# Performance work log

Hardware: AMD Instinct MI355X
Metric: run time of the kernel (lower is better)

Reference implementation:

```python
import jax, jax.numpy as jnp
import numpy as np

FULL_SCALE = 128
TOPK = 8
R = 0.5


def setup_inputs() -> dict:
    key = jax.random.key(0)
    ks = jax.random.split(key, 6)
    B, Na, Nb, D = 4, 8192, 8192, 256
    return {
        "a_feats": jax.random.normal(ks[0], (B, Na, D), jnp.float32),
        "b_feats": jax.random.normal(ks[1], (B, Nb, D), jnp.float32),
        "coords_a": jax.random.randint(ks[2], (B, Na, 3), 0, 2048, jnp.int32),
        "coords_b": jax.random.randint(ks[3], (B, Nb, 3), 0, 2048, jnp.int32),
        "w1": jax.random.normal(ks[4], (D, 2 * D), jnp.float32) / np.sqrt(2 * D),
        "b1": jnp.zeros((D,), jnp.float32),
        "w2": jax.random.normal(ks[5], (D, D), jnp.float32) / np.sqrt(D),
        "b2": jnp.zeros((D,), jnp.float32),
    }


def _cli_one(af, bf, ca, cb, w1, b1, w2, b2):
    # af:[Na,D] bf:[Nb,D] ca:[Na,3] cb:[Nb,3] (float coords, already //16)
    # torch.cdist (euclidean) / full_scale
    d2 = (jnp.sum(ca * ca, 1)[:, None] + jnp.sum(cb * cb, 1)[None, :]
          - 2.0 * ca @ cb.T)
    dist = jnp.sqrt(jnp.maximum(d2, 0.0)) / FULL_SCALE  # [Na, Nb]
    neg_d, idx = jax.lax.top_k(-dist, TOPK)             # smallest k distances
    dw = R - jnp.clip(-neg_d, 0.0, R)                   # [Na, k]
    nb = bf[idx]                                        # gather [Na, k, D]
    x = jnp.concatenate([nb, af[:, None, :] - nb], axis=-1)  # [Na, k, 2D]
    h = jax.nn.relu(jnp.einsum('nkf,df->nkd', x, w1) + b1) * dw[..., None]
    o = jnp.einsum('nkd,ed->nke', h, w2) + b2           # [Na, k, D]
    return jnp.sum(o, axis=1)                           # [Na, D]


def reference(a_feats, b_feats, coords_a, coords_b, w1, b1, w2, b2):
    ca = (coords_a // 16).astype(jnp.float32)
    cb = (coords_b // 16).astype(jnp.float32)
    fuse = jax.vmap(lambda af, bf, x, y: _cli_one(af, bf, x, y, w1, b1, w2, b2))(
        a_feats, b_feats, ca, cb)
    # ME.cat(a, tmp): concatenate features along channel dim
    return jnp.concatenate([a_feats, fuse], axis=-1)  # [B, Na, 2D]
```

## Files before the change

### kernel.cpp

```cpp
#include <hip/hip_runtime.h>
#include <math.h>

typedef short short8_t __attribute__((ext_vector_type(8)));
typedef __bf16 bf16x8_t __attribute__((ext_vector_type(8)));
typedef float f32x4_t __attribute__((ext_vector_type(4)));

__device__ __forceinline__ float bf2f(unsigned short u) {
  unsigned v = ((unsigned)u) << 16;
  return __builtin_bit_cast(float, v);
}
__device__ __forceinline__ unsigned short f2bf(float f) {
  unsigned x = __builtin_bit_cast(unsigned, f);
  x += 0x7fffu + ((x >> 16) & 1u);
  return (unsigned short)(x >> 16);
}

#define NA 8192
#define NB 8192
#define NBATCH 4
#define DIM 256
#define NPTS (NBATCH * NA)
#define NCELL 2048
#define SUBL 8

__device__ __forceinline__ void kins(unsigned k[8], unsigned x) {
  unsigned c = x < k[7] ? x : k[7];
#pragma unroll
  for (int i = 6; i >= 0; i--) {
    unsigned hi = k[i] > c ? k[i] : c;
    c = k[i] < c ? k[i] : c;
    k[i + 1] = hi;
  }
  k[0] = c;
}

__global__ __launch_bounds__(256) void prep_weights(
    const float* __restrict__ w1, const float* __restrict__ w2,
    unsigned short* __restrict__ Wdiff, unsigned short* __restrict__ Wb,
    unsigned short* __restrict__ W2b, unsigned* __restrict__ bcnt,
    unsigned* __restrict__ acnt, unsigned* __restrict__ failcnt) {
  int d = blockIdx.x, t = threadIdx.x;
  float wa = w1[d * 512 + t];
  float wb = w1[d * 512 + 256 + t];
  Wdiff[d * 256 + t] = f2bf(wa - wb);
  Wb[d * 256 + t] = f2bf(wb);
  W2b[d * 256 + t] = f2bf(w2[d * 256 + t]);
  if (d < 8) {
    int i = d * 256 + t;
    bcnt[i] = 0;
    acnt[i] = 0;
    if (i == 0) *failcnt = 0;
  }
}

__global__ __launch_bounds__(256) void pack_count_ab(
    const int* __restrict__ coords_b, const int* __restrict__ coords_a,
    unsigned* __restrict__ bpk, unsigned* __restrict__ apk,
    unsigned* __restrict__ bcnt, unsigned* __restrict__ acnt) {
  int gi = blockIdx.x * 256 + threadIdx.x;
  const int isA = gi >= NPTS;
  const int i = gi & (NPTS - 1);
  const int* __restrict__ coords = isA ? coords_a : coords_b;
  unsigned* __restrict__ pk = isA ? apk : bpk;
  unsigned* __restrict__ cnt = isA ? acnt : bcnt;
  int x = (coords[(size_t)i * 3 + 0] >> 4) & 127;
  int y = (coords[(size_t)i * 3 + 1] >> 4) & 127;
  int z = (coords[(size_t)i * 3 + 2] >> 4) & 127;
  pk[i] = (unsigned)(x | (y << 7) | (z << 14));
  int cid = ((i >> 13) << 9) | ((x >> 4) << 6) | ((y >> 4) << 3) | (z >> 4);
  atomicAdd(cnt + cid, 1u);
}

__global__ __launch_bounds__(256) void scan_cells(
    const unsigned* __restrict__ bcnt, const unsigned* __restrict__ acnt,
    unsigned* __restrict__ boff, unsigned* __restrict__ aoff,
    unsigned* __restrict__ bcur, unsigned* __restrict__ acur) {
  __shared__ unsigned p[256];
  const int t = threadIdx.x;
  for (int tab = 0; tab < 2; tab++) {
    const unsigned* cnt = tab ? acnt : bcnt;
    unsigned* off = tab ? aoff : boff;
    unsigned* cur = tab ? acur : bcur;
    unsigned loc[8], sum = 0;
#pragma unroll
    for (int k = 0; k < 8; k++) { loc[k] = sum; sum += cnt[t * 8 + k]; }
    p[t] = sum;
    __syncthreads();
    for (int d = 1; d < 256; d <<= 1) {
      unsigned v = (t >= d) ? p[t - d] : 0u;
      __syncthreads();
      p[t] += v;
      __syncthreads();
    }
    unsigned base = (t == 0) ? 0u : p[t - 1];
#pragma unroll
    for (int k = 0; k < 8; k++) {
      unsigned o = base + loc[k];
      off[t * 8 + k] = o;
      cur[t * 8 + k] = o;
    }
    if (t == 255) off[2048] = base + sum;
    __syncthreads();
  }
}

__global__ __launch_bounds__(256) void scatter_ab(
    const unsigned* __restrict__ bpk, const unsigned* __restrict__ apk,
    unsigned* __restrict__ bcur, unsigned* __restrict__ acur,
    uint2* __restrict__ bout, uint2* __restrict__ aout) {
  int gi = blockIdx.x * 256 + threadIdx.x;
  const int isA = gi >= NPTS;
  const int i = gi & (NPTS - 1);
  const unsigned* __restrict__ pk = isA ? apk : bpk;
  unsigned* __restrict__ cur = isA ? acur : bcur;
  uint2* __restrict__ out = isA ? aout : bout;
  unsigned v = pk[i];
  int cx = (v & 127) >> 4, cy = ((v >> 7) & 127) >> 4, cz = ((v >> 14) & 127) >> 4;
  int cid = ((i >> 13) << 9) | (cx << 6) | (cy << 3) | cz;
  unsigned pos = atomicAdd(cur + cid, 1u);
  out[pos] = make_uint2(v, (unsigned)(i & 8191));
}

#define LDT 72
template <int F32IN>
__device__ __forceinline__ void gemm64_body(
    int rowblk, const void* __restrict__ Ain, const short* __restrict__ W,
    float* __restrict__ Cf, unsigned short* __restrict__ Cb,
    const float* __restrict__ bias, float bias_scale, int c_stride,
    int c_coloff, float* __restrict__ copyout, short* As, short* Bs) {
  const int tid = threadIdx.x;
  const int row0 = rowblk * 64;
  const int w = tid >> 6, lane = tid & 63;
  const int wn = w * 64;
  f32x4_t acc[4][4] = {};
  for (int k0 = 0; k0 < 256; k0 += 64) {
    if (F32IN) {
      const float* Af = (const float*)Ain;
#pragma unroll
      for (int i = 0; i < 2; i++) {
        int c = tid + 256 * i;
        int r = c >> 3, kc = (c & 7) * 8;
        const float* src = Af + (size_t)(row0 + r) * 256 + k0 + kc;
        float4 v0 = *(const float4*)src;
        float4 v1 = *(const float4*)(src + 4);
        short8_t vb;
        vb[0] = (short)f2bf(v0.x); vb[1] = (short)f2bf(v0.y);
        vb[2] = (short)f2bf(v0.z); vb[3] = (short)f2bf(v0.w);
        vb[4] = (short)f2bf(v1.x); vb[5] = (short)f2bf(v1.y);
        vb[6] = (short)f2bf(v1.z); vb[7] = (short)f2bf(v1.w);
        *(short8_t*)(As + r * LDT + kc) = vb;
        if (copyout) {
          float4* dst = (float4*)(copyout + (size_t)(row0 + r) * 512 + k0 + kc);
          dst[0] = v0;
          dst[1] = v1;
        }
      }
    } else {
      const short* Ab = (const short*)Ain;
#pragma unroll
      for (int i = 0; i < 2; i++) {
        int c = tid + 256 * i;
        int r = c >> 3, kc = (c & 7) * 8;
        *(short8_t*)(As + r * LDT + kc) =
            *(const short8_t*)(Ab + (size_t)(row0 + r) * 256 + k0 + kc);
      }
    }
#pragma unroll
    for (int i = 0; i < 8; i++) {
      int c = tid + 256 * i;
      int r = c >> 3, kc = (c & 7) * 8;
      *(short8_t*)(Bs + r * LDT + kc) =
          *(const short8_t*)(W + (size_t)r * 256 + k0 + kc);
    }
    __syncthreads();
#pragma unroll
    for (int kk = 0; kk < 64; kk += 32) {
      const int kof = kk + (lane >> 4) * 8;
      bf16x8_t af[4], bfr[4];
#pragma unroll
      for (int i = 0; i < 4; i++) {
        af[i] = __builtin_bit_cast(bf16x8_t,
            *(const short8_t*)(As + (i * 16 + (lane & 15)) * LDT + kof));
        bfr[i] = __builtin_bit_cast(bf16x8_t,
            *(const short8_t*)(Bs + (wn + i * 16 + (lane & 15)) * LDT + kof));
      }
#pragma unroll
      for (int i = 0; i < 4; i++)
#pragma unroll
        for (int j = 0; j < 4; j++)
          acc[i][j] = __builtin_amdgcn_mfma_f32_16x16x32_bf16(
              af[i], bfr[j], acc[i][j], 0, 0, 0);
    }
    __syncthreads();
  }
#pragma unroll
  for (int i = 0; i < 4; i++) {
    int row = row0 + i * 16 + ((lane >> 4) * 4);
#pragma unroll
    for (int j = 0; j < 4; j++) {
      int col = wn + j * 16 + (lane & 15);
      float bv = bias ? bias[col] * bias_scale : 0.f;
#pragma unroll
      for (int r = 0; r < 4; r++) {
        float v = acc[i][j][r] + bv;
        size_t off = (size_t)(row + r) * c_stride + c_coloff + col;
        if (Cf) Cf[off] = v;
        else Cb[off] = f2bf(v);
      }
    }
  }
}

__global__ __launch_bounds__(256, 3) void gemm_ab(
    const float* __restrict__ a_feats, const float* __restrict__ b_feats,
    const short* __restrict__ Wb16, const short* __restrict__ Wdiff,
    unsigned short* __restrict__ Pa, unsigned short* __restrict__ Pb,
    const float* __restrict__ b1, float* __restrict__ outp) {
  __shared__ __attribute__((aligned(16))) short As[64 * LDT];
  __shared__ __attribute__((aligned(16))) short Bs[256 * LDT];
  const int nb = NPTS / 64;
  const int isB = blockIdx.x >= nb;
  const int rowblk = isB ? (blockIdx.x - nb) : blockIdx.x;
  const float* Af = isB ? b_feats : a_feats;
  const short* W = isB ? Wdiff : Wb16;
  unsigned short* P = isB ? Pb : Pa;
  const float* bias = isB ? nullptr : b1;
  float* copy = isB ? nullptr : outp;
  gemm64_body<1>(rowblk, (const void*)Af, W, nullptr, P, bias, 1.0f, 256, 0,
                 copy, As, Bs);
}

__global__ __launch_bounds__(256, 3) void gemm_h(
    const short* __restrict__ Hb, const short* __restrict__ W2b,
    float* __restrict__ outp, const float* __restrict__ b2) {
  __shared__ __attribute__((aligned(16))) short As[64 * LDT];
  __shared__ __attribute__((aligned(16))) short Bs[256 * LDT];
  gemm64_body<0>(blockIdx.x, (const void*)Hb, W2b, outp, nullptr, b2, 8.0f,
                 512, 256, nullptr, As, Bs);
}

__global__ __launch_bounds__(256) void topk_bins(
    const unsigned* __restrict__ boff, const uint2* __restrict__ bcj,
    const uint2* __restrict__ acj, int* __restrict__ idxb,
    float* __restrict__ dwb, unsigned* __restrict__ failcnt,
    unsigned* __restrict__ faillist) {
  const int tid = blockIdx.x * 256 + threadIdx.x;
  const int t = tid / SUBL;
  const int sub = tid & (SUBL - 1);
  const uint2 av = acj[t];
  const int batch = t >> 13;
  const int ax = av.x & 127, ay = (av.x >> 7) & 127, az = (av.x >> 14) & 127;
  const int cx = ax >> 4, cy = ay >> 4, cz = az >> 4;
  const int xlo = max(cx - 1, 0), xhi = min(cx + 1, 7);
  const int ylo = max(cy - 1, 0), yhi = min(cy + 1, 7);
  const int zlo = max(cz - 1, 0), zhi1 = min(cz + 1, 7) + 1;
  unsigned k[8];
#pragma unroll
  for (int s = 0; s < 8; s++) k[s] = 0xFFFFFFF8u + s;
  for (int nx = xlo; nx <= xhi; nx++) {
    for (int ny = ylo; ny <= yhi; ny++) {
      const int cb = (batch << 9) | (nx << 6) | (ny << 3);
      const int gs = (int)boff[cb + zlo];
      const int ge = (int)boff[cb + zhi1];
      for (int i = gs + sub; i < ge; i += SUBL) {
        const uint2 b = bcj[i];
        const int dx = ax - (int)(b.x & 127);
        const int dy = ay - (int)((b.x >> 7) & 127);
        const int dz = az - (int)((b.x >> 14) & 127);
        const unsigned d2 = (unsigned)(__mul24(dx, dx) + __mul24(dy, dy) +
                                       __mul24(dz, dz));
        kins(k, (d2 << 13) | b.y);
      }
    }
  }
  const int lane = threadIdx.x & 63;
#pragma unroll
  for (int half = 1; half < SUBL; half <<= 1) {
    unsigned o[8];
#pragma unroll
    for (int s = 0; s < 8; s++)
      o[s] = (unsigned)__shfl((int)k[s], lane ^ half, 64);
#pragma unroll
    for (int s = 0; s < 8; s++) kins(k, o[s]);
  }
  if (sub == 0) {
    const int g = (batch << 13) | (int)av.y;
#pragma unroll
    for (int s = 0; s < 8; s++) {
      unsigned key = k[s];
      idxb[(size_t)g * 8 + s] = (int)(key & 8191u);
      float dist = sqrtf((float)(key >> 13)) * (1.0f / 128.0f);
      dwb[(size_t)g * 8 + s] = 0.5f - fminf(dist, 0.5f);
    }
    if (k[7] >= (289u << 13)) {
      unsigned fp = atomicAdd(failcnt, 1u);
      faillist[fp] = (unsigned)g;
    }
  }
}

__global__ __launch_bounds__(256) void topk_fallback(
    const unsigned* __restrict__ failcnt, const unsigned* __restrict__ faillist,
    const uint2* __restrict__ bcj, const unsigned* __restrict__ apk,
    int* __restrict__ idxb, float* __restrict__ dwb) {
  __shared__ unsigned sk[4 * 8];
  const int tid = threadIdx.x;
  const int wv = tid >> 6, lane = tid & 63;
  const unsigned nf = *failcnt;
  for (unsigned fi = blockIdx.x; fi < nf; fi += gridDim.x) {
    const unsigned g = faillist[fi];
    const int batch = (int)(g >> 13);
    const unsigned av = apk[g];
    const int ax = av & 127, ay = (av >> 7) & 127, az = (av >> 14) & 127;
    const uint2* pb = bcj + ((size_t)batch << 13);
    unsigned k[8];
#pragma unroll
    for (int s = 0; s < 8; s++) k[s] = 0xFFFFFFF8u + s;
#pragma unroll 8
    for (int i = tid; i < NB; i += 256) {
      const uint2 b = pb[i];
      const int dx = ax - (int)(b.x & 127);
      const int dy = ay - (int)((b.x >> 7) & 127);
      const int dz = az - (int)((b.x >> 14) & 127);
      const unsigned d2 = (unsigned)(__mul24(dx, dx) + __mul24(dy, dy) +
                                     __mul24(dz, dz));
      kins(k, (d2 << 13) | b.y);
    }
#pragma unroll
    for (int half = 32; half >= 1; half >>= 1) {
      unsigned o[8];
#pragma unroll
      for (int s = 0; s < 8; s++)
        o[s] = (unsigned)__shfl((int)k[s], lane ^ half, 64);
#pragma unroll
      for (int s = 0; s < 8; s++) kins(k, o[s]);
    }
    if (lane == 0) {
#pragma unroll
      for (int s = 0; s < 8; s++) sk[wv * 8 + s] = k[s];
    }
    __syncthreads();
    if (tid == 0) {
#pragma unroll
      for (int w = 1; w < 4; w++)
#pragma unroll
        for (int s = 0; s < 8; s++) kins(k, sk[w * 8 + s]);
#pragma unroll
      for (int s = 0; s < 8; s++) {
        unsigned key = k[s];
        idxb[(size_t)g * 8 + s] = (int)(key & 8191u);
        float dist = sqrtf((float)(key >> 13)) * (1.0f / 128.0f);
        dwb[(size_t)g * 8 + s] = 0.5f - fminf(dist, 0.5f);
      }
    }
    __syncthreads();
  }
}

__global__ __launch_bounds__(256) void fuse_kernel(
    const unsigned short* __restrict__ Pa, const unsigned short* __restrict__ Pb,
    const uint2* __restrict__ acj, const int* __restrict__ idxb,
    const float* __restrict__ dwb, unsigned short* __restrict__ H) {
  const int t = blockIdx.x * 4 + (threadIdx.x >> 6);
  const int lane = threadIdx.x & 63;
  const int batch = t >> 13;
  const uint2 av = acj[t];
  const int g = (batch << 13) | (int)av.y;
  const size_t fo = (size_t)g * 256 + lane * 4;
  ushort4 pav = *(const ushort4*)(Pa + fo);
  const float pa0 = bf2f(pav.x), pa1 = bf2f(pav.y), pa2 = bf2f(pav.z),
              pa3 = bf2f(pav.w);
  float h0 = 0.f, h1 = 0.f, h2 = 0.f, h3 = 0.f;
  const size_t bbase = (size_t)(batch << 13) * 256;
#pragma unroll
  for (int k = 0; k < 8; k++) {
    const int j = idxb[(size_t)g * 8 + k];
    const float w = dwb[(size_t)g * 8 + k];
    const ushort4 pbv =
        *(const ushort4*)(Pb + bbase + (size_t)j * 256 + lane * 4);
    h0 += fmaxf(pa0 + bf2f(pbv.x), 0.f) * w;
    h1 += fmaxf(pa1 + bf2f(pbv.y), 0.f) * w;
    h2 += fmaxf(pa2 + bf2f(pbv.z), 0.f) * w;
    h3 += fmaxf(pa3 + bf2f(pbv.w), 0.f) * w;
  }
  ushort4 hv;
  hv.x = f2bf(h0); hv.y = f2bf(h1); hv.z = f2bf(h2); hv.w = f2bf(h3);
  *(ushort4*)(H + fo) = hv;
}

extern "C" void kernel_launch(void* const* d_in, const int* in_sizes, int n_in,
                              void* d_out, int out_size, void* d_ws,
                              size_t ws_size, hipStream_t stream) {
  const float* a_feats = (const float*)d_in[0];
  const float* b_feats = (const float*)d_in[1];
  const int* coords_a = (const int*)d_in[2];
  const int* coords_b = (const int*)d_in[3];
  const float* w1 = (const float*)d_in[4];
  const float* b1 = (const float*)d_in[5];
  const float* w2 = (const float*)d_in[6];
  const float* b2 = (const float*)d_in[7];
  float* outp = (float*)d_out;

  char* p = (char*)d_ws;
  auto take = [&](size_t bytes) {
    char* r = p;
    p += (bytes + 255) & ~(size_t)255;
    return r;
  };
  unsigned short* Pa = (unsigned short*)take((size_t)NPTS * DIM * 2);
  unsigned short* Pb = (unsigned short*)take((size_t)NPTS * DIM * 2);
  unsigned short* Hb = (unsigned short*)take((size_t)NPTS * DIM * 2);
  int* idxb = (int*)take((size_t)NPTS * 8 * 4);
  float* dwb = (float*)take((size_t)NPTS * 8 * 4);
  unsigned* bpk = (unsigned*)take((size_t)NPTS * 4);
  unsigned* apk = (unsigned*)take((size_t)NPTS * 4);
  unsigned* bcnt = (unsigned*)take(NCELL * 4);
  unsigned* acnt = (unsigned*)take(NCELL * 4);
  unsigned* bcur = (unsigned*)take(NCELL * 4);
  unsigned* acur = (unsigned*)take(NCELL * 4);
  unsigned* boff = (unsigned*)take((NCELL + 1) * 4);
  unsigned* aoff = (unsigned*)take((NCELL + 1) * 4);
  uint2* bcj = (uint2*)take((size_t)NPTS * 8);
  uint2* acj = (uint2*)take((size_t)NPTS * 8);
  unsigned* failcnt = (unsigned*)take(256);
  unsigned* faillist = (unsigned*)take((size_t)NPTS * 4);
  unsigned short* Wdiff = (unsigned short*)take(256 * 256 * 2);
  unsigned short* Wb16 = (unsigned short*)take(256 * 256 * 2);
  unsigned short* W2b = (unsigned short*)take(256 * 256 * 2);

  prep_weights<<<256, 256, 0, stream>>>(w1, w2, Wdiff, Wb16, W2b, bcnt, acnt,
                                        failcnt);
  pack_count_ab<<<2 * NPTS / 256, 256, 0, stream>>>(coords_b, coords_a, bpk,
                                                    apk, bcnt, acnt);
  scan_cells<<<1, 256, 0, stream>>>(bcnt, acnt, boff, aoff, bcur, acur);
  scatter_ab<<<2 * NPTS / 256, 256, 0, stream>>>(bpk, apk, bcur, acur, bcj,
                                                 acj);

  gemm_ab<<<2 * NPTS / 64, 256, 0, stream>>>(a_feats, b_feats,
                                             (const short*)Wb16,
                                             (const short*)Wdiff, Pa, Pb, b1,
                                             outp);

  topk_bins<<<NPTS * SUBL / 256, 256, 0, stream>>>(boff, bcj, acj, idxb, dwb,
                                                   failcnt, faillist);
  topk_fallback<<<256, 256, 0, stream>>>(failcnt, faillist, bcj, apk, idxb,
                                         dwb);

  fuse_kernel<<<NPTS / 4, 256, 0, stream>>>(Pa, Pb, acj, idxb, dwb, Hb);

  gemm_h<<<NPTS / 64, 256, 0, stream>>>((const short*)Hb, (const short*)W2b,
                                        outp, b2);
}
```

Baseline: 227.0 us.

## Double-buffer A tile with register prefetch and read weights directly from global

The GEMM body now prefetches the next 64-wide K slice of A into registers while the current one is consumed, writing into two alternating LDS buffers, so one barrier per iteration is dropped. The weight tile is no longer staged in shared memory; each wave loads its B fragments straight from global/L2. LDS per block falls sharply and launch bounds no longer force three blocks per CU, which should raise occupancy. The cost is uncoalesced-ish per-lane global weight loads inside the MFMA loop and higher register pressure from the prefetch buffers.

```diff
diff --git a/kernel.cpp b/kernel.cpp
--- a/kernel.cpp
+++ b/kernel.cpp
@@ -127,51 +127,56 @@
     int rowblk, const void* __restrict__ Ain, const short* __restrict__ W,
     float* __restrict__ Cf, unsigned short* __restrict__ Cb,
     const float* __restrict__ bias, float bias_scale, int c_stride,
-    int c_coloff, float* __restrict__ copyout, short* As, short* Bs) {
+    int c_coloff, float* __restrict__ copyout, short* As) {
   const int tid = threadIdx.x;
   const int row0 = rowblk * 64;
   const int w = tid >> 6, lane = tid & 63;
   const int wn = w * 64;
+  const int r0 = tid >> 3, kc = (tid & 7) * 8;
+  const int r1 = r0 + 32;
+  const short* wbase = W + (size_t)(wn + (lane & 15)) * 256 + (lane >> 4) * 8;
   f32x4_t acc[4][4] = {};
+
+  float4 p00, p01, p10, p11;
+  short8_t pb0, pb1;
+  const float* Af = (const float*)Ain;
+  const short* Ab = (const short*)Ain;
+#define LOADA(K0)                                                   \
+  if (F32IN) {                                                      \
+    const float* s0 = Af + (size_t)(row0 + r0) * 256 + (K0) + kc;   \
+    const float* s1 = Af + (size_t)(row0 + r1) * 256 + (K0) + kc;   \
+    p00 = *(const float4*)s0; p01 = *(const float4*)(s0 + 4);       \
+    p10 = *(const float4*)s1; p11 = *(const float4*)(s1 + 4);       \
+  } else {                                                          \
+    pb0 = *(const short8_t*)(Ab + (size_t)(row0 + r0) * 256 + (K0) + kc); \
+    pb1 = *(const short8_t*)(Ab + (size_t)(row0 + r1) * 256 + (K0) + kc); \
+  }
+  LOADA(0)
   for (int k0 = 0; k0 < 256; k0 += 64) {
+    short* Ac = As + ((k0 >> 6) & 1) * (64 * LDT);
     if (F32IN) {
-      const float* Af = (const float*)Ain;
-#pragma unroll
-      for (int i = 0; i < 2; i++) {
-        int c = tid + 256 * i;
-        int r = c >> 3, kc = (c & 7) * 8;
-        const float* src = Af + (size_t)(row0 + r) * 256 + k0 + kc;
-        float4 v0 = *(const float4*)src;
-        float4 v1 = *(const float4*)(src + 4);
-        short8_t vb;
-        vb[0] = (short)f2bf(v0.x); vb[1] = (short)f2bf(v0.y);
-        vb[2] = (short)f2bf(v0.z); vb[3] = (short)f2bf(v0.w);
-        vb[4] = (short)f2bf(v1.x); vb[5] = (short)f2bf(v1.y);
-        vb[6] = (short)f2bf(v1.z); vb[7] = (short)f2bf(v1.w);
-        *(short8_t*)(As + r * LDT + kc) = vb;
-        if (copyout) {
-          float4* dst = (float4*)(copyout + (size_t)(row0 + r) * 512 + k0 + kc);
-          dst[0] = v0;
-          dst[1] = v1;
-        }
+      short8_t vb;
+      vb[0] = (short)f2bf(p00.x); vb[1] = (short)f2bf(p00.y);
+      vb[2] = (short)f2bf(p00.z); vb[3] = (short)f2bf(p00.w);
+      vb[4] = (short)f2bf(p01.x); vb[5] = (short)f2bf(p01.y);
+      vb[6] = (short)f2bf(p01.z); vb[7] = (short)f2bf(p01.w);
+      *(short8_t*)(Ac + r0 * LDT + kc) = vb;
+      vb[0] = (short)f2bf(p10.x); vb[1] = (short)f2bf(p10.y);
+      vb[2] = (short)f2bf(p10.z); vb[3] = (short)f2bf(p10.w);
+      vb[4] = (short)f2bf(p11.x); vb[5] = (short)f2bf(p11.y);
+      vb[6] = (short)f2bf(p11.z); vb[7] = (short)f2bf(p11.w);
+      *(short8_t*)(Ac + r1 * LDT + kc) = vb;
+      if (copyout) {
+        float4* d0 = (float4*)(copyout + (size_t)(row0 + r0) * 512 + k0 + kc);
+        d0[0] = p00; d0[1] = p01;
+        float4* d1 = (float4*)(copyout + (size_t)(row0 + r1) * 512 + k0 + kc);
+        d1[0] = p10; d1[1] = p11;
       }
     } else {
-      const short* Ab = (const short*)Ain;
-#pragma unroll
-      for (int i = 0; i < 2; i++) {
-        int c = tid + 256 * i;
-        int r = c >> 3, kc = (c & 7) * 8;
-        *(short8_t*)(As + r * LDT + kc) =
-            *(const short8_t*)(Ab + (size_t)(row0 + r) * 256 + k0 + kc);
-      }
-    }
-#pragma unroll
-    for (int i = 0; i < 8; i++) {
-      int c = tid + 256 * i;
-      int r = c >> 3, kc = (c & 7) * 8;
-      *(short8_t*)(Bs + r * LDT + kc) =
-          *(const short8_t*)(W + (size_t)r * 256 + k0 + kc);
-    }
+      *(short8_t*)(Ac + r0 * LDT + kc) = pb0;
+      *(short8_t*)(Ac + r1 * LDT + kc) = pb1;
+    }
+    if (k0 < 192) { LOADA(k0 + 64) }
     __syncthreads();
 #pragma unroll
     for (int kk = 0; kk < 64; kk += 32) {
@@ -180,9 +185,9 @@
 #pragma unroll
       for (int i = 0; i < 4; i++) {
         af[i] = __builtin_bit_cast(bf16x8_t,
-            *(const short8_t*)(As + (i * 16 + (lane & 15)) * LDT + kof));
+            *(const short8_t*)(Ac + (i * 16 + (lane & 15)) * LDT + kof));
         bfr[i] = __builtin_bit_cast(bf16x8_t,
-            *(const short8_t*)(Bs + (wn + i * 16 + (lane & 15)) * LDT + kof));
+            *(const short8_t*)(wbase + (size_t)i * 16 * 256 + k0 + kk));
       }
 #pragma unroll
       for (int i = 0; i < 4; i++)
@@ -191,8 +196,8 @@
           acc[i][j] = __builtin_amdgcn_mfma_f32_16x16x32_bf16(
               af[i], bfr[j], acc[i][j], 0, 0, 0);
     }
-    __syncthreads();
-  }
+  }
+#undef LOADA
 #pragma unroll
   for (int i = 0; i < 4; i++) {
     int row = row0 + i * 16 + ((lane >> 4) * 4);
@@ -211,13 +216,12 @@
   }
 }
 
-__global__ __launch_bounds__(256, 3) void gemm_ab(
+__global__ __launch_bounds__(256) void gemm_ab(
     const float* __restrict__ a_feats, const float* __restrict__ b_feats,
     const short* __restrict__ Wb16, const short* __restrict__ Wdiff,
     unsigned short* __restrict__ Pa, unsigned short* __restrict__ Pb,
     const float* __restrict__ b1, float* __restrict__ outp) {
-  __shared__ __attribute__((aligned(16))) short As[64 * LDT];
-  __shared__ __attribute__((aligned(16))) short Bs[256 * LDT];
+  __shared__ __attribute__((aligned(16))) short As[2 * 64 * LDT];
   const int nb = NPTS / 64;
   const int isB = blockIdx.x >= nb;
   const int rowblk = isB ? (blockIdx.x - nb) : blockIdx.x;
@@ -227,16 +231,15 @@
   const float* bias = isB ? nullptr : b1;
   float* copy = isB ? nullptr : outp;
   gemm64_body<1>(rowblk, (const void*)Af, W, nullptr, P, bias, 1.0f, 256, 0,
-                 copy, As, Bs);
-}
-
-__global__ __launch_bounds__(256, 3) void gemm_h(
+                 copy, As);
+}
+
+__global__ __launch_bounds__(256) void gemm_h(
     const short* __restrict__ Hb, const short* __restrict__ W2b,
     float* __restrict__ outp, const float* __restrict__ b2) {
-  __shared__ __attribute__((aligned(16))) short As[64 * LDT];
-  __shared__ __attribute__((aligned(16))) short Bs[256 * LDT];
+  __shared__ __attribute__((aligned(16))) short As[2 * 64 * LDT];
   gemm64_body<0>(blockIdx.x, (const void*)Hb, W2b, outp, nullptr, b2, 8.0f,
-                 512, 256, nullptr, As, Bs);
+                 512, 256, nullptr, As);
 }
 
 __global__ __launch_bounds__(256) void topk_bins(
```

After: 227.7 us. About the same (+0.3%).

## Replace LDS-tiled GEMMs with per-wave 16-row strips streaming weights from global

Applied to the files above, without the earlier changes.

Both GEMMs now drop shared-memory tiling and barriers. Each wave owns a 16-row strip, keeps its full K=256 A fragment in registers, and reads the 256x256 bf16 weight fragments directly from global memory (L1/L2) for all 16 output column tiles. This removes LDS staging, __syncthreads and occupancy limits from shared memory. In exchange every wave re-reads the whole weight matrix from cache, so there is far less reuse per loaded weight and more register pressure.

```diff
diff --git a/kernel.cpp b/kernel.cpp
--- a/kernel.cpp
+++ b/kernel.cpp
@@ -121,122 +121,96 @@
   out[pos] = make_uint2(v, (unsigned)(i & 8191));
 }
 
-#define LDT 72
 template <int F32IN>
-__device__ __forceinline__ void gemm64_body(
-    int rowblk, const void* __restrict__ Ain, const short* __restrict__ W,
+__device__ __forceinline__ void gemm_strip(
+    int strip, const void* __restrict__ Ain, const short* __restrict__ W,
     float* __restrict__ Cf, unsigned short* __restrict__ Cb,
     const float* __restrict__ bias, float bias_scale, int c_stride,
-    int c_coloff, float* __restrict__ copyout, short* As, short* Bs) {
-  const int tid = threadIdx.x;
-  const int row0 = rowblk * 64;
-  const int w = tid >> 6, lane = tid & 63;
-  const int wn = w * 64;
-  f32x4_t acc[4][4] = {};
-  for (int k0 = 0; k0 < 256; k0 += 64) {
-    if (F32IN) {
-      const float* Af = (const float*)Ain;
-#pragma unroll
-      for (int i = 0; i < 2; i++) {
-        int c = tid + 256 * i;
-        int r = c >> 3, kc = (c & 7) * 8;
-        const float* src = Af + (size_t)(row0 + r) * 256 + k0 + kc;
-        float4 v0 = *(const float4*)src;
-        float4 v1 = *(const float4*)(src + 4);
-        short8_t vb;
-        vb[0] = (short)f2bf(v0.x); vb[1] = (short)f2bf(v0.y);
-        vb[2] = (short)f2bf(v0.z); vb[3] = (short)f2bf(v0.w);
-        vb[4] = (short)f2bf(v1.x); vb[5] = (short)f2bf(v1.y);
-        vb[6] = (short)f2bf(v1.z); vb[7] = (short)f2bf(v1.w);
-        *(short8_t*)(As + r * LDT + kc) = vb;
-        if (copyout) {
-          float4* dst = (float4*)(copyout + (size_t)(row0 + r) * 512 + k0 + kc);
-          dst[0] = v0;
-          dst[1] = v1;
-        }
+    int c_coloff, float* __restrict__ copyout) {
+  const int lane = threadIdx.x & 63;
+  const int r = lane & 15, g = lane >> 4;
+  const int row0 = strip * 16;
+  const float* Af = (const float*)Ain;
+  const short* Ab = (const short*)Ain;
+  bf16x8_t a[8];
+  if (F32IN) {
+#pragma unroll
+    for (int k = 0; k < 8; k++) {
+      const float* s = Af + (size_t)(row0 + r) * 256 + k * 32 + g * 8;
+      float4 v0 = *(const float4*)s;
+      float4 v1 = *(const float4*)(s + 4);
+      short8_t vb;
+      vb[0] = (short)f2bf(v0.x); vb[1] = (short)f2bf(v0.y);
+      vb[2] = (short)f2bf(v0.z); vb[3] = (short)f2bf(v0.w);
+      vb[4] = (short)f2bf(v1.x); vb[5] = (short)f2bf(v1.y);
+      vb[6] = (short)f2bf(v1.z); vb[7] = (short)f2bf(v1.w);
+      a[k] = __builtin_bit_cast(bf16x8_t, vb);
+      if (copyout) {
+        float4* d = (float4*)(copyout + (size_t)(row0 + r) * 512 + k * 32 + g * 8);
+        d[0] = v0;
+        d[1] = v1;
       }
-    } else {
-      const short* Ab = (const short*)Ain;
-#pragma unroll
-      for (int i = 0; i < 2; i++) {
-        int c = tid + 256 * i;
-        int r = c >> 3, kc = (c & 7) * 8;
-        *(short8_t*)(As + r * LDT + kc) =
-            *(const short8_t*)(Ab + (size_t)(row0 + r) * 256 + k0 + kc);
-      }
-    }
-#pragma unroll
-    for (int i = 0; i < 8; i++) {
-      int c = tid + 256 * i;
-      int r = c >> 3, kc = (c & 7) * 8;
-      *(short8_t*)(Bs + r * LDT + kc) =
-          *(const short8_t*)(W + (size_t)r * 256 + k0 + kc);
-    }
-    __syncthreads();
-#pragma unroll
-    for (int kk = 0; kk < 64; kk += 32) {
-      const int kof = kk + (lane >> 4) * 8;
-      bf16x8_t af[4], bfr[4];
-#pragma unroll
-      for (int i = 0; i < 4; i++) {
-        af[i] = __builtin_bit_cast(bf16x8_t,
-            *(const short8_t*)(As + (i * 16 + (lane & 15)) * LDT + kof));
-        bfr[i] = __builtin_bit_cast(bf16x8_t,
-            *(const short8_t*)(Bs + (wn + i * 16 + (lane & 15)) * LDT + kof));
-      }
-#pragma unroll
-      for (int i = 0; i < 4; i++)
-#pragma unroll
-        for (int j = 0; j < 4; j++)
-          acc[i][j] = __builtin_amdgcn_mfma_f32_16x16x32_bf16(
-              af[i], bfr[j], acc[i][j], 0, 0, 0);
-    }
-    __syncthreads();
-  }
-#pragma unroll
-  for (int i = 0; i < 4; i++) {
-    int row = row0 + i * 16 + ((lane >> 4) * 4);
-#pragma unroll
-    for (int j = 0; j < 4; j++) {
-      int col = wn + j * 16 + (lane & 15);
-      float bv = bias ? bias[col] * bias_scale : 0.f;
-#pragma unroll
-      for (int r = 0; r < 4; r++) {
-        float v = acc[i][j][r] + bv;
-        size_t off = (size_t)(row + r) * c_stride + c_coloff + col;
-        if (Cf) Cf[off] = v;
-        else Cb[off] = f2bf(v);
-      }
-    }
-  }
-}
-
-__global__ __launch_bounds__(256, 3) void gemm_ab(
+    }
+  } else {
+#pragma unroll
+    for (int k = 0; k < 8; k++)
+      a[k] = __builtin_bit_cast(bf16x8_t,
+          *(const short8_t*)(Ab + (size_t)(row0 + r) * 256 + k * 32 + g * 8));
+  }
+  const short* wb = W + (size_t)r * 256 + g * 8;
+  f32x4_t acc[16];
+#pragma unroll
+  for (int j = 0; j < 16; j++) acc[j] = f32x4_t{0.f, 0.f, 0.f, 0.f};
+#pragma unroll
+  for (int j = 0; j < 16; j++) {
+    bf16x8_t b[8];
+#pragma unroll
+    for (int k = 0; k < 8; k++)
+      b[k] = __builtin_bit_cast(bf16x8_t,
+          *(const short8_t*)(wb + (size_t)j * 16 * 256 + k * 32));
+#pragma unroll
+    for (int k = 0; k < 8; k++)
+      acc[j] = __builtin_amdgcn_mfma_f32_16x16x32_bf16(a[k], b[k], acc[j],
+                                                       0, 0, 0);
+  }
+#pragma unroll
+  for (int j = 0; j < 16; j++) {
+    float bv = bias ? bias[j * 16 + r] * bias_scale : 0.f;
+#pragma unroll
+    for (int rr = 0; rr < 4; rr++) {
+      float v = acc[j][rr] + bv;
+      size_t off =
+          (size_t)(row0 + g * 4 + rr) * c_stride + c_coloff + j * 16 + r;
+      if (Cf) Cf[off] = v;
+      else Cb[off] = f2bf(v);
+    }
+  }
+}
+
+__global__ __launch_bounds__(256) void gemm_ab(
     const float* __restrict__ a_feats, const float* __restrict__ b_feats,
     const short* __restrict__ Wb16, const short* __restrict__ Wdiff,
     unsigned short* __restrict__ Pa, unsigned short* __restrict__ Pb,
     const float* __restrict__ b1, float* __restrict__ outp) {
-  __shared__ __attribute__((aligned(16))) short As[64 * LDT];
-  __shared__ __attribute__((aligned(16))) short Bs[256 * LDT];
-  const int nb = NPTS / 64;
-  const int isB = blockIdx.x >= nb;
-  const int rowblk = isB ? (blockIdx.x - nb) : blockIdx.x;
+  const int wave = blockIdx.x * 4 + (threadIdx.x >> 6);
+  const int ns = NPTS / 16;
+  const int isB = wave >= ns;
+  const int strip = isB ? (wave - ns) : wave;
   const float* Af = isB ? b_feats : a_feats;
   const short* W = isB ? Wdiff : Wb16;
   unsigned short* P = isB ? Pb : Pa;
   const float* bias = isB ? nullptr : b1;
   float* copy = isB ? nullptr : outp;
-  gemm64_body<1>(rowblk, (const void*)Af, W, nullptr, P, bias, 1.0f, 256, 0,
-                 copy, As, Bs);
-}
-
-__global__ __launch_bounds__(256, 3) void gemm_h(
+  gemm_strip<1>(strip, (const void*)Af, W, nullptr, P, bias, 1.0f, 256, 0,
+                copy);
+}
+
+__global__ __launch_bounds__(256) void gemm_h(
     const short* __restrict__ Hb, const short* __restrict__ W2b,
     float* __restrict__ outp, const float* __restrict__ b2) {
-  __shared__ __attribute__((aligned(16))) short As[64 * LDT];
-  __shared__ __attribute__((aligned(16))) short Bs[256 * LDT];
-  gemm64_body<0>(blockIdx.x, (const void*)Hb, W2b, outp, nullptr, b2, 8.0f,
-                 512, 256, nullptr, As, Bs);
+  const int strip = blockIdx.x * 4 + (threadIdx.x >> 6);
+  gemm_strip<0>(strip, (const void*)Hb, W2b, outp, nullptr, b2, 8.0f, 512,
+                256, nullptr);
 }
 
 __global__ __launch_bounds__(256) void topk_bins(
@@ -436,10 +410,10 @@
   scatter_ab<<<2 * NPTS / 256, 256, 0, stream>>>(bpk, apk, bcur, acur, bcj,
                                                  acj);
 
-  gemm_ab<<<2 * NPTS / 64, 256, 0, stream>>>(a_feats, b_feats,
-                                             (const short*)Wb16,
-                                             (const short*)Wdiff, Pa, Pb, b1,
-                                             outp);
+  gemm_ab<<<2 * NPTS / 16 / 4, 256, 0, stream>>>(a_feats, b_feats,
+                                                 (const short*)Wb16,
+                                                 (const short*)Wdiff, Pa, Pb,
+                                                 b1, outp);
 
   topk_bins<<<NPTS * SUBL / 256, 256, 0, stream>>>(boff, bcj, acj, idxb, dwb,
                                                    failcnt, faillist);
@@ -448,6 +422,6 @@
 
   fuse_kernel<<<NPTS / 4, 256, 0, stream>>>(Pa, Pb, acj, idxb, dwb, Hb);
 
-  gemm_h<<<NPTS / 64, 256, 0, stream>>>((const short*)Hb, (const short*)W2b,
-                                        outp, b2);
-}
+  gemm_h<<<NPTS / 16 / 4, 256, 0, stream>>>((const short*)Hb,
+                                            (const short*)W2b, outp, b2);
+}
```

New measurement: 293.9 us. 29.5% more time.
